# Optimization experiments

Measured on AMD Instinct MI355X. Metric: run time of the kernel, lower is better.

The kernel has to match this reference:

```python
import jax, jax.numpy as jnp
import numpy as np

B, T, E, H, L, V = 16, 512, 512, 8, 4, 2048
HS = E // H  # head_size = n_embd // n_head
FF = 4 * E


def _ln(x, g, b):
    m = x.mean(-1, keepdims=True)
    v = ((x - m) ** 2).mean(-1, keepdims=True)
    return (x - m) * jax.lax.rsqrt(v + 1e-5) * g + b


def setup_inputs() -> dict:
    key = jax.random.key(0)
    ks = jax.random.split(key, 16)
    s = jnp.float32(0.02)
    return {
        "idx": jax.random.randint(ks[0], (B, T), 0, V),
        "tok_emb": jax.random.normal(ks[1], (V, E), jnp.float32) * s,
        "pos_emb": jax.random.normal(ks[2], (T, E), jnp.float32) * s,
        "Wq": jax.random.normal(ks[3], (L, E, E), jnp.float32) * s,
        "Wk": jax.random.normal(ks[4], (L, E, E), jnp.float32) * s,
        "Wv": jax.random.normal(ks[5], (L, E, E), jnp.float32) * s,
        "rel": jax.random.normal(ks[6], (L, 2 * T - 1, HS), jnp.float32) * s,
        "Wo": jax.random.normal(ks[7], (L, E, E), jnp.float32) * s,
        "bo": jnp.zeros((L, E), jnp.float32),
        "ln1_g": jnp.ones((L, E), jnp.float32),
        "ln1_b": jnp.zeros((L, E), jnp.float32),
        "W1": jax.random.normal(ks[8], (L, E, FF), jnp.float32) * s,
        "b1": jnp.zeros((L, FF), jnp.float32),
        "W2": jax.random.normal(ks[9], (L, FF, E), jnp.float32) * s,
        "b2": jnp.zeros((L, E), jnp.float32),
        "ln2_g": jnp.ones((L, E), jnp.float32),
        "ln2_b": jnp.zeros((L, E), jnp.float32),
        "lnf_g": jnp.ones((E,), jnp.float32),
        "lnf_b": jnp.zeros((E,), jnp.float32),
        "Wlm": jax.random.normal(ks[10], (E, V), jnp.float32) * s,
        "blm": jnp.zeros((V,), jnp.float32),
    }


def reference(idx, tok_emb, pos_emb, Wq, Wk, Wv, rel, Wo, bo, ln1_g, ln1_b,
              W1, b1, W2, b2, ln2_g, ln2_b, lnf_g, lnf_b, Wlm, blm):
    x = tok_emb[idx] + pos_emb[None, :T]  # (B,T,E)
    ri = jnp.arange(T)
    rel_idx = ri[:, None] - ri[None, :] + (T - 1)  # block_size == T
    causal = ri[:, None] >= ri[None, :]            # (T,T) lower-triangular
    scale = jnp.float32(1.0 / np.sqrt(HS))
    for l in range(L):
        h = _ln(x, ln1_g[l], ln1_b[l])
        # NOTE: torch code does .view(B, H, T, HS) on a (B, T, H*HS) tensor
        # (NOT a transpose) -- jnp.reshape matches row-major view semantics.
        q = (h @ Wq[l]).reshape(B, H, T, HS)
        k = (h @ Wk[l]).reshape(B, H, T, HS)
        v = (h @ Wv[l]).reshape(B, H, T, HS)
        re = rel[l][rel_idx]  # (T,T,HS)
        # rel scores: sum_d q[b,h,i,d]*re[i,j,d]; avoid the 5D intermediate
        scores = jnp.einsum('bhid,bhjd->bhij', q, k) * scale \
               + jnp.einsum('bhid,ijd->bhij', q, re)
        scores = jnp.where(causal, scores, -jnp.inf)
        att = jax.nn.softmax(scores, axis=-1)  # dropout disabled (eval)
        ctx = jnp.einsum('bhij,bhjd->bhid', att, v)
        ctx = jnp.swapaxes(ctx, 1, 2).reshape(B, T, H * HS)
        x = x + ctx @ Wo[l] + bo[l]
        h2 = _ln(x, ln2_g[l], ln2_b[l])
        x = x + jax.nn.relu(h2 @ W1[l] + b1[l]) @ W2[l] + b2[l]
    x = _ln(x, lnf_g, lnf_b)
    return x @ Wlm + blm  # logits (B,T,V)
```

## Files before the change

### kernel.cpp

```cpp
#include <hip/hip_runtime.h>
#include <hip/hip_bf16.h>
#include <stdint.h>

typedef __hip_bfloat16 bf16;
typedef __attribute__((ext_vector_type(8))) short bf16x8;
typedef __attribute__((ext_vector_type(8))) short short8;
typedef __attribute__((ext_vector_type(4))) float f32x4;

#define DEV __device__ __forceinline__

static constexpr int Bn = 16, Tn = 512, En = 512, Hn = 8, Ln = 4, Vn = 2048;
static constexpr int HSn = 64, FFn = 2048, Mn = Bn * Tn;
static constexpr int SQ = 1536;

DEV f32x4 mfma16(bf16x8 a, bf16x8 b, f32x4 c) {
  return __builtin_amdgcn_mfma_f32_16x16x32_bf16(a, b, c, 0, 0, 0);
}
DEV float b2f(bf16 x) { return __bfloat162float(x); }
DEV bf16 f2b(float x) { return __float2bfloat16(x); }
DEV short f2s(float x) { bf16 h = f2b(x); return reinterpret_cast<short&>(h); }

DEV void gload16(const void* g, void* l) {
  __builtin_amdgcn_global_load_lds(
      (const __attribute__((address_space(1))) void*)(uintptr_t)g,
      (__attribute__((address_space(3))) void*)(uint32_t)(uintptr_t)l, 16, 0, 0);
}

__global__ __launch_bounds__(256) void ktranspose(const float* __restrict__ in,
                                                  bf16* __restrict__ out, int R, int C,
                                                  long in_zs, long out_zs) {
  __shared__ float tile[32][33];
  int z = blockIdx.z;
  const float* inz = in + (size_t)z * in_zs;
  bf16* outz = out + (size_t)z * out_zs;
  int c0 = blockIdx.x * 32, r0 = blockIdx.y * 32;
  for (int k = 0; k < 32; k += 8)
    tile[threadIdx.y + k][threadIdx.x] =
        inz[(size_t)(r0 + threadIdx.y + k) * C + (c0 + threadIdx.x)];
  __syncthreads();
  for (int k = 0; k < 32; k += 8)
    outz[(size_t)(c0 + threadIdx.y + k) * R + (r0 + threadIdx.x)] =
        f2b(tile[threadIdx.x][threadIdx.y + k]);
}

__global__ __launch_bounds__(256) void kcast(const float* __restrict__ in,
                                             bf16* __restrict__ out, int n) {
  int i = blockIdx.x * 256 + threadIdx.x;
  if (i < n) out[i] = f2b(in[i]);
}

__global__ __launch_bounds__(256) void kembed(const int* __restrict__ idx,
                                              const float* __restrict__ tok,
                                              const float* __restrict__ pos,
                                              float* __restrict__ x) {
  int i = blockIdx.x * 256 + threadIdx.x;
  int e4 = (i & 127) * 4;
  int bt = i >> 7;
  int t = bt & (Tn - 1);
  f32x4 tv = *(const f32x4*)(tok + (size_t)idx[bt] * En + e4);
  f32x4 pv = *(const f32x4*)(pos + (size_t)t * En + e4);
  *(f32x4*)(x + (size_t)bt * En + e4) = tv + pv;
}

__global__ __launch_bounds__(256) void kln(const float* __restrict__ x,
                                           const float* __restrict__ g,
                                           const float* __restrict__ b,
                                           bf16* __restrict__ out) {
  int row = blockIdx.x * 4 + (threadIdx.x >> 6);
  int lane = threadIdx.x & 63;
  const float* xr = x + (size_t)row * En + lane * 8;
  f32x4 a0 = *(const f32x4*)xr;
  f32x4 a1 = *(const f32x4*)(xr + 4);
  float s = a0[0] + a0[1] + a0[2] + a0[3] + a1[0] + a1[1] + a1[2] + a1[3];
  for (int m = 1; m < 64; m <<= 1) s += __shfl_xor(s, m);
  float mean = s * (1.f / En);
  float s2 = 0.f;
  for (int j = 0; j < 4; j++) { float d0 = a0[j] - mean, d1 = a1[j] - mean; s2 += d0 * d0 + d1 * d1; }
  for (int m = 1; m < 64; m <<= 1) s2 += __shfl_xor(s2, m);
  float rstd = rsqrtf(s2 * (1.f / En) + 1e-5f);
  f32x4 g0 = *(const f32x4*)(g + lane * 8), g1 = *(const f32x4*)(g + lane * 8 + 4);
  f32x4 b0 = *(const f32x4*)(b + lane * 8), b1 = *(const f32x4*)(b + lane * 8 + 4);
  short8 ov;
  for (int j = 0; j < 4; j++) {
    ov[j] = f2s((a0[j] - mean) * rstd * g0[j] + b0[j]);
    ov[j + 4] = f2s((a1[j] - mean) * rstd * g1[j] + b1[j]);
  }
  *(short8*)(out + (size_t)row * En + lane * 8) = ov;
}

template <int BM, int BN, int TW, int DB, int SWZ, int NBIAS, int RELU, int MODE>
__global__ __launch_bounds__(TW) void kgemm(const bf16* __restrict__ A,
                                            const bf16* __restrict__ Bt,
                                            const float* __restrict__ bias,
                                            float* __restrict__ outf,
                                            bf16* __restrict__ outh, int Ndim, int K) {
  constexpr int NW = TW / 64;
  constexpr int WCN = NW / 2;
  constexpr int WM = BM / 2, WN = BN / WCN, MI = WM / 16, NI = WN / 16;
  constexpr int NB = DB ? 2 : 1;
  __shared__ bf16 As[NB][BM * 64];
  __shared__ bf16 Bs[NB][BN * 64];
  int t = threadIdx.x, lane = t & 63, w = t >> 6;
  int lr = lane & 15, lg = lane >> 4;
  int sx = lr & 7;
  int wr = w / WCN, wc = w % WCN;
  int bx, by;
  if (SWZ) {
    int id = blockIdx.x + gridDim.x * blockIdx.y;
    int xcd = id & 7, s = id >> 3;
    int gx = gridDim.x;
    by = xcd * 8 + s / gx;
    bx = s % gx;
  } else {
    bx = blockIdx.x; by = blockIdx.y;
  }
  int br = by * BM, bc = bx * BN;
  f32x4 acc[MI][NI] = {};
  int rl = lane >> 3, cb = (lane & 7) ^ rl;
  const bf16* Abase = A + (size_t)(br + w * (BM / NW) + rl) * K + cb * 8;
  const bf16* Bbase = Bt + (size_t)(bc + w * (BN / NW) + rl) * K + cb * 8;

  auto STAGE = [&](int buf, int kt) {
    for (int c = 0; c < BM / (8 * NW); c++)
      gload16(Abase + (size_t)(c * 8) * K + kt, &As[buf][(w * (BM / NW) + c * 8) * 64]);
    for (int c = 0; c < BN / (8 * NW); c++)
      gload16(Bbase + (size_t)(c * 8) * K + kt, &Bs[buf][(w * (BN / NW) + c * 8) * 64]);
  };
  auto COMPUTE = [&](int buf) {
    for (int kk = 0; kk < 2; kk++) {
      int gb = (kk * 4 + lg) ^ sx;
      bf16x8 af[MI], bfr[NI];
      for (int mi = 0; mi < MI; mi++)
        af[mi] = *(const bf16x8*)&As[buf][(wr * WM + mi * 16 + lr) * 64 + gb * 8];
      for (int ni = 0; ni < NI; ni++)
        bfr[ni] = *(const bf16x8*)&Bs[buf][(wc * WN + ni * 16 + lr) * 64 + gb * 8];
      for (int mi = 0; mi < MI; mi++)
        for (int ni = 0; ni < NI; ni++)
          acc[mi][ni] = mfma16(af[mi], bfr[ni], acc[mi][ni]);
    }
  };

  if (DB) {
    STAGE(0, 0);
    __syncthreads();
    int nt = K / 64;
    for (int t2 = 0; t2 < nt; t2++) {
      int cur = t2 & 1;
      if (t2 + 1 < nt) STAGE(cur ^ 1, (t2 + 1) * 64);
      COMPUTE(cur);
      __syncthreads();
    }
  } else {
    for (int kt = 0; kt < K; kt += 64) {
      __syncthreads();
      STAGE(0, kt);
      __syncthreads();
      COMPUTE(0);
    }
  }

  for (int mi = 0; mi < MI; mi++)
    for (int ni = 0; ni < NI; ni++)
      for (int r = 0; r < 4; r++) {
        int row = br + wr * WM + mi * 16 + lg * 4 + r;
        int col = bc + wc * WN + ni * 16 + lr;
        float val = acc[mi][ni][r];
        if (NBIAS) val += bias[col];
        if (RELU) val = fmaxf(val, 0.f);
        if (MODE == 1) outf[(size_t)row * Ndim + col] += val;
        else if (MODE == 2) outf[(size_t)row * Ndim + col] = val;
        else outh[(size_t)row * Ndim + col] = f2b(val);
      }
}

template <int NBIAS, int RELU, int MODE>
__global__ __launch_bounds__(512) void kgemm8(const bf16* __restrict__ A,
                                              const bf16* __restrict__ Bt,
                                              const float* __restrict__ bias,
                                              float* __restrict__ outf,
                                              bf16* __restrict__ outh, int Ndim, int K) {
  __shared__ bf16 As[2][256 * 64];
  __shared__ bf16 Bs[2][256 * 64];
  int t = threadIdx.x, lane = t & 63, w = t >> 6;
  int lr = lane & 15, lg = lane >> 4;
  int sx = lr & 7;
  int wr = w >> 2, wc = w & 3;
  int rl8 = lane >> 3, cb = (lane & 7) ^ rl8;
  int id = blockIdx.x + gridDim.x * blockIdx.y;
  int xcd = id & 7, s = id >> 3;
  int by = xcd * 4 + (s >> 3), bx = s & 7;
  int br = by * 256, bc = bx * 256;
  f32x4 acc[8][4] = {};
  const bf16* Abase = A + (size_t)(br + w * 16 + rl8) * K + cb * 8;
  const bf16* Bbase = Bt + (size_t)(bc + w * 16 + rl8) * K + cb * 8;

  auto STAGEH = [&](int hh, int buf, int kt) {
    int half = hh & 1;
    if (hh < 2) {
      const bf16* g = Abase + (size_t)(half * 128) * K + kt;
      bf16* l = &As[buf][(half * 128 + w * 16) * 64];
      gload16(g, l);
      gload16(g + (size_t)8 * K, l + 8 * 64);
    } else {
      const bf16* g = Bbase + (size_t)(half * 128) * K + kt;
      bf16* l = &Bs[buf][(half * 128 + w * 16) * 64];
      gload16(g, l);
      gload16(g + (size_t)8 * K, l + 8 * 64);
    }
  };

#define PHASE8(Q, P)                                                          \
  do {                                                                        \
    constexpr int mh = (Q) >> 1, nh = (Q) & 1;                                \
    bf16x8 af[4][2], bfr[2][2];                                               \
    _Pragma("unroll") for (int kk = 0; kk < 2; kk++) {                        \
      int gb = (kk * 4 + lg) ^ sx;                                            \
      _Pragma("unroll") for (int i = 0; i < 4; i++)                           \
        af[i][kk] = *(const bf16x8*)&As[P][(wr * 128 + (mh * 4 + i) * 16 + lr) * 64 + gb * 8]; \
      _Pragma("unroll") for (int j = 0; j < 2; j++)                           \
        bfr[j][kk] = *(const bf16x8*)&Bs[P][(wc * 64 + (nh * 2 + j) * 16 + lr) * 64 + gb * 8]; \
    }                                                                         \
    __builtin_amdgcn_s_setprio(1);                                            \
    _Pragma("unroll") for (int i = 0; i < 4; i++)                             \
      _Pragma("unroll") for (int j = 0; j < 2; j++) {                         \
        acc[mh * 4 + i][nh * 2 + j] =                                         \
            mfma16(af[i][0], bfr[j][0], acc[mh * 4 + i][nh * 2 + j]);         \
        acc[mh * 4 + i][nh * 2 + j] =                                         \
            mfma16(af[i][1], bfr[j][1], acc[mh * 4 + i][nh * 2 + j]);         \
      }                                                                       \
    __builtin_amdgcn_s_setprio(0);                                            \
  } while (0)

  int nt = K / 64;
  for (int hh = 0; hh < 4; hh++) STAGEH(hh, 0, 0);
  STAGEH(0, 1, 64);
  STAGEH(1, 1, 64);
  asm volatile("s_waitcnt vmcnt(4)" ::: "memory");
  asm volatile("s_barrier" ::: "memory");
  for (int t2 = 0; t2 < nt; t2++) {
    int p = t2 & 1;
    if (t2 + 1 < nt) STAGEH(2, p ^ 1, (t2 + 1) * 64);
    PHASE8(0, p);
    if (t2 + 1 < nt) STAGEH(3, p ^ 1, (t2 + 1) * 64);
    PHASE8(1, p);
    PHASE8(2, p);
    PHASE8(3, p);
    asm volatile("s_barrier" ::: "memory");
    if (t2 + 2 < nt) {
      STAGEH(0, p, (t2 + 2) * 64);
      STAGEH(1, p, (t2 + 2) * 64);
      asm volatile("s_waitcnt vmcnt(4)" ::: "memory");
      asm volatile("s_barrier" ::: "memory");
    } else if (t2 + 1 < nt) {
      asm volatile("s_waitcnt vmcnt(0)" ::: "memory");
      asm volatile("s_barrier" ::: "memory");
    }
  }
#undef PHASE8
#pragma unroll
  for (int mi = 0; mi < 8; mi++)
#pragma unroll
    for (int ni = 0; ni < 4; ni++)
#pragma unroll
      for (int r = 0; r < 4; r++) {
        int row = br + wr * 128 + mi * 16 + lg * 4 + r;
        int col = bc + wc * 64 + ni * 16 + lr;
        float val = acc[mi][ni][r];
        if (NBIAS) val += bias[col];
        if (RELU) val = fmaxf(val, 0.f);
        if (MODE == 2) outf[(size_t)row * Ndim + col] = val;
        else outh[(size_t)row * Ndim + col] = f2b(val);
      }
}

__global__ __launch_bounds__(512) void kattn(const bf16* __restrict__ qkv,
                                             const bf16* __restrict__ rel,
                                             bf16* __restrict__ ctx) {
  __shared__ bf16 Ks[128 * 64];
  __shared__ bf16 Vs[64 * 128];
  __shared__ bf16 Prel[8][16 * 81];
  __shared__ bf16 Ps[8][16 * 64];
  int pairp = blockIdx.x, bh = blockIdx.y;
  int b = bh >> 3, hh = bh & 7;
  int t = threadIdx.x, lane = t & 63, w = t >> 6;
  int wl = w & 3, wg = w >> 2;
  int lr = lane & 15, lg = lane >> 4;
  int sx = lr & 7;
  int rl8 = lane >> 3, cbk = (lane & 7) ^ rl8;
  const size_t headrow = (size_t)(b * Tn + hh * 64);
  bf16* prw = &Prel[w][0];
  bf16* psw = &Ps[w][0];
  int jp = t >> 3, db = (t & 7) * 8;

  int ia = pairp, ib = 7 - pairp;
  int myblk = wg ? ia : ib;
  int mylast = myblk * 64;
  int i0w = myblk * 64 + wl * 16;
  bf16x8 aq[2];
  {
    int t2 = i0w + lr;
    const bf16* qp = qkv + (headrow + (t2 >> 3)) * SQ + (t2 & 7) * 64;
    aq[0] = *(const bf16x8*)(qp + lg * 8);
    aq[1] = *(const bf16x8*)(qp + 32 + lg * 8);
  }
  f32x4 o[4] = {};
  float m_run = -3e38f, l_run = 0.f;
  int ntiles = (ib >> 1) + 1;

  auto SUBTILE = [&](int jb, bool diag, int su) {
    int njmax = diag ? wl : 3;
    int nmmin = diag ? 3 - wl : 0;
    __builtin_amdgcn_s_setprio(1);
    f32x4 sqk[4] = {};
    for (int nj = 0; nj <= njmax; nj++) {
      int row = su * 64 + nj * 16 + lr;
      bf16x8 kb0 = *(const bf16x8*)&Ks[row * 64 + ((lg ^ sx) * 8)];
      bf16x8 kb1 = *(const bf16x8*)&Ks[row * 64 + (((4 + lg) ^ sx) * 8)];
      sqk[nj] = mfma16(kb0, aq[0], sqk[nj]);
      sqk[nj] = mfma16(kb1, aq[1], sqk[nj]);
    }
    int base = i0w - jb + 448;
    for (int nm = nmmin; nm < 5; nm++) {
      int mrow = base + nm * 16 + lr;
      if (mrow > 1022) mrow = 1022;
      const bf16* rp = rel + (size_t)mrow * 64;
      f32x4 sr = {};
      sr = mfma16(aq[0], *(const bf16x8*)(rp + lg * 8), sr);
      sr = mfma16(aq[1], *(const bf16x8*)(rp + 32 + lg * 8), sr);
      for (int r = 0; r < 4; r++)
        prw[(lg * 4 + r) * 81 + nm * 16 + lr] = f2b(sr[r]);
    }
    __builtin_amdgcn_s_setprio(0);
    float sv[4][4];
    for (int nj = 0; nj < 4; nj++)
      for (int r = 0; r < 4; r++) sv[nj][r] = -3e38f;
    float mloc = -3e38f;
    for (int nj = 0; nj <= njmax; nj++)
      for (int r = 0; r < 4; r++) {
        int jj = nj * 16 + lg * 4 + r;
        float val = sqk[nj][r] * 0.125f + b2f(prw[lr * 81 + (lr - jj + 63)]);
        if (jb + jj > i0w + lr) val = -3e38f;
        sv[nj][r] = val;
        mloc = fmaxf(mloc, val);
      }
    mloc = fmaxf(mloc, __shfl_xor(mloc, 16));
    mloc = fmaxf(mloc, __shfl_xor(mloc, 32));
    float mnew = fmaxf(m_run, mloc);
    float corr = __expf(m_run - mnew);
    m_run = mnew;
    float lsum = 0.f;
    for (int nj = 0; nj < 4; nj++)
      for (int r = 0; r < 4; r++) {
        float p = __expf(sv[nj][r] - mnew);
        lsum += p;
        psw[lr * 64 + (((nj * 2 + (lg >> 1)) ^ sx) * 8) + (lg & 1) * 4 + r] = f2b(p);
      }
    lsum += __shfl_xor(lsum, 16);
    lsum += __shfl_xor(lsum, 32);
    l_run = l_run * corr + lsum;
    for (int r = 0; r < 4; r++) {
      float c = __shfl(corr, lg * 4 + r);
      for (int nd = 0; nd < 4; nd++) o[nd][r] *= c;
    }
    __builtin_amdgcn_s_setprio(1);
    bf16x8 ap0 = *(const bf16x8*)&psw[lr * 64 + ((lg ^ sx) * 8)];
    bf16x8 ap1 = *(const bf16x8*)&psw[lr * 64 + (((4 + lg) ^ sx) * 8)];
    for (int nd = 0; nd < 4; nd++) {
      int d = nd * 16 + lr;
      bf16x8 vb0 = *(const bf16x8*)&Vs[d * 128 + ((su * 8 + (lg ^ sx)) * 8)];
      bf16x8 vb1 = *(const bf16x8*)&Vs[d * 128 + ((su * 8 + ((4 + lg) ^ sx)) * 8)];
      o[nd] = mfma16(ap0, vb0, o[nd]);
      o[nd] = mfma16(ap1, vb1, o[nd]);
    }
    __builtin_amdgcn_s_setprio(0);
  };

  for (int jt = 0; jt < ntiles; jt++) {
    int jbase = jt * 128;
    bf16x8 vv[2];
#pragma unroll
    for (int u = 0; u < 2; u++) {
      int j0 = jbase + jp * 2 + u;
      vv[u] = *(const bf16x8*)(qkv + (headrow + (j0 >> 3)) * SQ + (j0 & 7) * 64 + 1024 + db);
    }
    __syncthreads();
#pragma unroll
    for (int c = 0; c < 2; c++) {
      int row = w * 16 + c * 8 + rl8;
      const bf16* src = qkv + (headrow + ((jbase + row) >> 3)) * SQ +
                        (row & 7) * 64 + 512 + cbk * 8;
      gload16(src, &Ks[(w * 16 + c * 8) * 64]);
    }
    {
      const short* pa = (const short*)&vv[0];
      const short* pb = (const short*)&vv[1];
      int j0 = jp * 2;
      int jblk = j0 >> 3, jin = j0 & 7;
#pragma unroll
      for (int u = 0; u < 8; u++) {
        int d = db + u;
        int idx = d * 128 + ((jblk ^ (d & 7)) * 8) + jin;
        uint32_t pk = (uint32_t)(uint16_t)pa[u] | ((uint32_t)(uint16_t)pb[u] << 16);
        *(uint32_t*)((short*)Vs + idx) = pk;
      }
    }
    __syncthreads();
#pragma unroll
    for (int su = 0; su < 2; su++) {
      int jb = jbase + su * 64;
      if (jb > ib * 64) break;
      if (jb <= mylast) SUBTILE(jb, jb == mylast, su);
    }
  }
  for (int r = 0; r < 4; r++) {
    float linv = 1.f / __shfl(l_run, lg * 4 + r);
    int row = i0w + lg * 4 + r;
    for (int nd = 0; nd < 4; nd++)
      ctx[((size_t)b * Tn + row) * En + hh * 64 + nd * 16 + lr] = f2b(o[nd][r] * linv);
  }
}

extern "C" void kernel_launch(void* const* d_in, const int* in_sizes, int n_in,
                              void* d_out, int out_size, void* d_ws, size_t ws_size,
                              hipStream_t stream) {
  (void)in_sizes; (void)n_in; (void)out_size; (void)ws_size;
  const int* idx = (const int*)d_in[0];
  const float* tok = (const float*)d_in[1];
  const float* pos = (const float*)d_in[2];
  const float* Wq = (const float*)d_in[3];
  const float* Wk = (const float*)d_in[4];
  const float* Wv = (const float*)d_in[5];
  const float* rel = (const float*)d_in[6];
  const float* Wo = (const float*)d_in[7];
  const float* bo = (const float*)d_in[8];
  const float* ln1_g = (const float*)d_in[9];
  const float* ln1_b = (const float*)d_in[10];
  const float* W1 = (const float*)d_in[11];
  const float* b1 = (const float*)d_in[12];
  const float* W2 = (const float*)d_in[13];
  const float* b2 = (const float*)d_in[14];
  const float* ln2_g = (const float*)d_in[15];
  const float* ln2_b = (const float*)d_in[16];
  const float* lnf_g = (const float*)d_in[17];
  const float* lnf_b = (const float*)d_in[18];
  const float* Wlm = (const float*)d_in[19];
  const float* blm = (const float*)d_in[20];

  char* ws = (char*)d_ws;
  float* x = (float*)(ws + 0);
  bf16* h = (bf16*)(ws + 16777216);
  bf16* qkv = (bf16*)(ws + 25165824);
  bf16* ctx = (bf16*)(ws + 50331648);
  bf16* ffn1 = qkv;
  bf16* wqkvT = (bf16*)(ws + 58720256);
  bf16* woT = wqkvT + (size_t)Ln * SQ * En;
  bf16* w1T = woT + (size_t)Ln * En * En;
  bf16* w2T = w1T + (size_t)Ln * En * FFn;
  bf16* wlmT = w2T + (size_t)Ln * FFn * En;
  bf16* relc = wlmT + (size_t)En * Vn;
  float* outf = (float*)d_out;

  dim3 tb(32, 8);
  ktranspose<<<dim3(16, 16, Ln), tb, 0, stream>>>(Wq, wqkvT, En, En, (long)En * En, (long)SQ * En);
  ktranspose<<<dim3(16, 16, Ln), tb, 0, stream>>>(Wk, wqkvT + 512 * 512, En, En, (long)En * En, (long)SQ * En);
  ktranspose<<<dim3(16, 16, Ln), tb, 0, stream>>>(Wv, wqkvT + 2 * 512 * 512, En, En, (long)En * En, (long)SQ * En);
  ktranspose<<<dim3(16, 16, Ln), tb, 0, stream>>>(Wo, woT, En, En, (long)En * En, (long)En * En);
  ktranspose<<<dim3(64, 16, Ln), tb, 0, stream>>>(W1, w1T, En, FFn, (long)En * FFn, (long)En * FFn);
  ktranspose<<<dim3(16, 64, Ln), tb, 0, stream>>>(W2, w2T, FFn, En, (long)FFn * En, (long)FFn * En);
  ktranspose<<<dim3(64, 16, 1), tb, 0, stream>>>(Wlm, wlmT, En, Vn, 0, 0);
  kcast<<<(Ln * (2 * Tn - 1) * HSn + 255) / 256, 256, 0, stream>>>(
      rel, relc, Ln * (2 * Tn - 1) * HSn);

  kembed<<<(Mn * En / 4) / 256, 256, 0, stream>>>(idx, tok, pos, x);

  for (int l = 0; l < Ln; l++) {
    kln<<<Mn / 4, 256, 0, stream>>>(x, ln1_g + (size_t)l * En, ln1_b + (size_t)l * En, h);
    kgemm<128, 128, 256, 0, 1, 0, 0, 0><<<dim3(12, 64), 256, 0, stream>>>(
        h, wqkvT + (size_t)l * SQ * En, nullptr, nullptr, qkv, SQ, En);
    kattn<<<dim3(4, 128), 512, 0, stream>>>(
        qkv, relc + (size_t)l * (2 * Tn - 1) * HSn, ctx);
    kgemm<128, 128, 512, 1, 1, 1, 0, 1><<<dim3(4, 64), 512, 0, stream>>>(
        ctx, woT + (size_t)l * En * En, bo + (size_t)l * En, x, nullptr, En, En);
    kln<<<Mn / 4, 256, 0, stream>>>(x, ln2_g + (size_t)l * En, ln2_b + (size_t)l * En, h);
    kgemm8<1, 1, 0><<<dim3(8, 32), 512, 0, stream>>>(
        h, w1T + (size_t)l * En * FFn, b1 + (size_t)l * FFn, nullptr, ffn1, FFn, En);
    kgemm<128, 128, 512, 1, 1, 1, 0, 1><<<dim3(4, 64), 512, 0, stream>>>(
        ffn1, w2T + (size_t)l * FFn * En, b2 + (size_t)l * En, x, nullptr, En, FFn);
  }
  kln<<<Mn / 4, 256, 0, stream>>>(x, lnf_g, lnf_b, h);
  kgemm8<1, 0, 2><<<dim3(8, 32), 512, 0, stream>>>(
      h, wlmT, blm, outf, nullptr, Vn, En);
}
```

Measured before the change: 630.3 us.

## Double-buffer K tiles and prefetch V in attention kernel

The attention kernel now keeps two K tiles in shared memory. While the current tile is being computed, it issues the async global-to-LDS load for the next K tile and a register prefetch of the next V tile, replacing the serial load-sync-compute loop. The per-warp Prel and Ps scratch buffers are merged into one array so the extra K buffer fits in shared memory. Full `__syncthreads` calls are replaced with raw `s_barrier` and an `lgkmcnt` wait. This relies on the compiler's `vmcnt` waits for the prefetched V registers to also cover completion of the async K loads, and on Prel and Ps reads and writes never overlapping within a warp.

After: 695.8 us. 1.1x slower.

```diff
diff --git a/kernel.cpp b/kernel.cpp
--- a/kernel.cpp
+++ b/kernel.cpp
@@ -276,10 +276,9 @@
 __global__ __launch_bounds__(512) void kattn(const bf16* __restrict__ qkv,
                                              const bf16* __restrict__ rel,
                                              bf16* __restrict__ ctx) {
-  __shared__ bf16 Ks[128 * 64];
+  __shared__ bf16 Ks[2][128 * 64];
   __shared__ bf16 Vs[64 * 128];
-  __shared__ bf16 Prel[8][16 * 81];
-  __shared__ bf16 Ps[8][16 * 64];
+  __shared__ bf16 PP[8][16 * 81];
   int pairp = blockIdx.x, bh = blockIdx.y;
   int b = bh >> 3, hh = bh & 7;
   int t = threadIdx.x, lane = t & 63, w = t >> 6;
@@ -288,8 +287,8 @@
   int sx = lr & 7;
   int rl8 = lane >> 3, cbk = (lane & 7) ^ rl8;
   const size_t headrow = (size_t)(b * Tn + hh * 64);
-  bf16* prw = &Prel[w][0];
-  bf16* psw = &Ps[w][0];
+  bf16* prw = &PP[w][0];
+  bf16* psw = &PP[w][0];
   int jp = t >> 3, db = (t & 7) * 8;
 
   int ia = pairp, ib = 7 - pairp;
@@ -307,15 +306,32 @@
   float m_run = -3e38f, l_run = 0.f;
   int ntiles = (ib >> 1) + 1;
 
-  auto SUBTILE = [&](int jb, bool diag, int su) {
+  auto KSTAGE = [&](int jbase, int buf) {
+#pragma unroll
+    for (int c = 0; c < 2; c++) {
+      int row = w * 16 + c * 8 + rl8;
+      const bf16* src = qkv + (headrow + ((jbase + row) >> 3)) * SQ +
+                        (row & 7) * 64 + 512 + cbk * 8;
+      gload16(src, &Ks[buf][(w * 16 + c * 8) * 64]);
+    }
+  };
+  auto VLOAD = [&](int jbase, bf16x8* v) {
+#pragma unroll
+    for (int u = 0; u < 2; u++) {
+      int j0 = jbase + jp * 2 + u;
+      v[u] = *(const bf16x8*)(qkv + (headrow + (j0 >> 3)) * SQ + (j0 & 7) * 64 + 1024 + db);
+    }
+  };
+
+  auto SUBTILE = [&](const bf16* ks, int jb, bool diag, int su) {
     int njmax = diag ? wl : 3;
     int nmmin = diag ? 3 - wl : 0;
     __builtin_amdgcn_s_setprio(1);
     f32x4 sqk[4] = {};
     for (int nj = 0; nj <= njmax; nj++) {
       int row = su * 64 + nj * 16 + lr;
-      bf16x8 kb0 = *(const bf16x8*)&Ks[row * 64 + ((lg ^ sx) * 8)];
-      bf16x8 kb1 = *(const bf16x8*)&Ks[row * 64 + (((4 + lg) ^ sx) * 8)];
+      bf16x8 kb0 = *(const bf16x8*)&ks[row * 64 + ((lg ^ sx) * 8)];
+      bf16x8 kb1 = *(const bf16x8*)&ks[row * 64 + (((4 + lg) ^ sx) * 8)];
       sqk[nj] = mfma16(kb0, aq[0], sqk[nj]);
       sqk[nj] = mfma16(kb1, aq[1], sqk[nj]);
     }
@@ -375,21 +391,16 @@
     __builtin_amdgcn_s_setprio(0);
   };
 
+  bf16x8 vv[2], nvv[2];
+  KSTAGE(0, 0);
+  VLOAD(0, vv);
+
   for (int jt = 0; jt < ntiles; jt++) {
-    int jbase = jt * 128;
-    bf16x8 vv[2];
-#pragma unroll
-    for (int u = 0; u < 2; u++) {
-      int j0 = jbase + jp * 2 + u;
-      vv[u] = *(const bf16x8*)(qkv + (headrow + (j0 >> 3)) * SQ + (j0 & 7) * 64 + 1024 + db);
-    }
-    __syncthreads();
-#pragma unroll
-    for (int c = 0; c < 2; c++) {
-      int row = w * 16 + c * 8 + rl8;
-      const bf16* src = qkv + (headrow + ((jbase + row) >> 3)) * SQ +
-                        (row & 7) * 64 + 512 + cbk * 8;
-      gload16(src, &Ks[(w * 16 + c * 8) * 64]);
+    int cur = jt & 1;
+    asm volatile("s_barrier" ::: "memory");
+    if (jt + 1 < ntiles) {
+      KSTAGE((jt + 1) * 128, cur ^ 1);
+      VLOAD((jt + 1) * 128, nvv);
     }
     {
       const short* pa = (const short*)&vv[0];
@@ -404,13 +415,17 @@
         *(uint32_t*)((short*)Vs + idx) = pk;
       }
     }
-    __syncthreads();
+    asm volatile("s_waitcnt lgkmcnt(0)" ::: "memory");
+    asm volatile("s_barrier" ::: "memory");
+    int jbase = jt * 128;
 #pragma unroll
     for (int su = 0; su < 2; su++) {
       int jb = jbase + su * 64;
       if (jb > ib * 64) break;
-      if (jb <= mylast) SUBTILE(jb, jb == mylast, su);
-    }
+      if (jb <= mylast) SUBTILE(&Ks[cur][0], jb, jb == mylast, su);
+    }
+    vv[0] = nvv[0];
+    vv[1] = nvv[1];
   }
   for (int r = 0; r < 4; r++) {
     float linv = 1.f / __shfl(l_run, lg * 4 + r);
```
